# Optimization experiments

Measured on AMD Instinct MI355X. Metric: run time of the kernel, lower is better.

The kernel has to match this reference:

```python
import jax, jax.numpy as jnp
import numpy as np

N_NODES = 50000
N_EDGES = 800000
IN_FEAT = 256
DIM_H = 64
DIM_OUT = 64


def setup_inputs() -> dict:
    key = jax.random.key(0)
    ks = jax.random.split(key, 9)
    x = jax.random.normal(ks[0], (N_NODES, IN_FEAT), dtype=jnp.float32)
    edge_index = jax.random.randint(ks[1], (2, N_EDGES), 0, N_NODES, dtype=jnp.int64)
    s_in = 1.0 / np.sqrt(IN_FEAT)
    s_h = 1.0 / np.sqrt(DIM_H)
    W_src = jax.random.normal(ks[2], (IN_FEAT, DIM_H), dtype=jnp.float32) * s_in
    W_dst = jax.random.normal(ks[3], (IN_FEAT, DIM_H), dtype=jnp.float32) * s_in
    att_src = jax.random.normal(ks[4], (DIM_H,), dtype=jnp.float32) * s_h
    att_dst = jax.random.normal(ks[5], (DIM_H,), dtype=jnp.float32) * s_h
    bias_conv = jax.random.normal(ks[6], (DIM_H,), dtype=jnp.float32) * 0.01
    W_lin = jax.random.normal(ks[7], (DIM_H, DIM_OUT), dtype=jnp.float32) * s_h
    b_lin = jax.random.normal(ks[8], (DIM_OUT,), dtype=jnp.float32) * 0.01
    return {"x": x, "edge_index": edge_index, "W_src": W_src, "W_dst": W_dst,
            "att_src": att_src, "att_dst": att_dst, "bias_conv": bias_conv,
            "W_lin": W_lin, "b_lin": b_lin}


def reference(x, edge_index, W_src, W_dst, att_src, att_dst, bias_conv, W_lin, b_lin):
    N = x.shape[0]
    src, dst = edge_index[0], edge_index[1]
    # linear projections (GATConv lin_src / lin_dst, no bias)
    h_src = x @ W_src                      # [N, H]
    h_dst = x @ W_dst                      # [N, H]
    # per-node attention logits
    a_src = h_src @ att_src                # [N]
    a_dst = h_dst @ att_dst                # [N]
    # edge-wise score: leaky_relu(a_src[src] + a_dst[dst])
    e = jax.nn.leaky_relu(a_src[src] + a_dst[dst], negative_slope=0.2)  # [E]
    # segment softmax over destination neighborhoods
    e_max = jax.ops.segment_max(e, dst, num_segments=N)
    e_exp = jnp.exp(e - e_max[dst])
    denom = jax.ops.segment_sum(e_exp, dst, num_segments=N)
    alpha = e_exp / denom[dst]             # [E]
    # weighted scatter-add aggregation
    msg = h_src[src] * alpha[:, None]      # [E, H]
    out = jax.ops.segment_sum(msg, dst, num_segments=N) + bias_conv  # [N, H]
    h = jax.nn.relu(out)
    return h @ W_lin + b_lin               # [N, dim_out]
```

## Files before the change

### kernel.cpp

```cpp
#include <hip/hip_runtime.h>
#include <math.h>

#define N_NODES 50000
#define N_EDGES 800000
#define IN_FEAT 256
#define DIM_H   64
#define NPAD    50176
#define CAP     48
#define NBUK    392
#define BNODES  128
#define BCAP    3072
#define EPB     4096
#define PBLKS   391
#define ABLKS   196
#define SPLIT   4
#define PNODES  32

typedef __attribute__((ext_vector_type(8)))  short  s16x8;
typedef __attribute__((ext_vector_type(16))) float  f32x16;

__device__ __forceinline__ float bcast_f(float v, int k) {
  return __int_as_float(__builtin_amdgcn_readlane(__float_as_int(v), k));
}
__device__ __forceinline__ short f2bf(float f) {
  unsigned u = __float_as_uint(f);
  u += 0x7fffu + ((u >> 16) & 1u);
  return (short)(u >> 16);
}

__global__ __launch_bounds__(256) void proj_binA_kernel(
    const float* __restrict__ x,
    const float* __restrict__ Wsrc,
    const float* __restrict__ Wdst,
    const float* __restrict__ att_src,
    const float* __restrict__ att_dst,
    const int* __restrict__ ei,
    unsigned* __restrict__ hbf,
    float* __restrict__ a_src,
    float* __restrict__ a_dst,
    int* __restrict__ gbc,
    unsigned* __restrict__ binbuf) {
  __shared__ short wfrag[16 * 2 * 64 * 8];
  __shared__ float wdl[IN_FEAT];
  __shared__ float attl[DIM_H];

  const int tid = threadIdx.x;

  if (blockIdx.x >= PBLKS) {
    int* bcnt = (int*)wfrag;
    int* wcur = bcnt + NBUK;
    const int e0 = (blockIdx.x - PBLKS) * EPB;

    for (int b = tid; b < NBUK; b += 256) bcnt[b] = 0;
    __syncthreads();

    int dst[16];
    #pragma unroll
    for (int i = 0; i < 16; ++i) {
      int e = e0 + tid + 256 * i;
      dst[i] = (e < N_EDGES) ? ei[N_EDGES + e] : -1;
      if (dst[i] >= 0) atomicAdd(&bcnt[dst[i] >> 7], 1);
    }
    __syncthreads();

    for (int b = tid; b < NBUK; b += 256) {
      int c = bcnt[b];
      wcur[b] = c ? atomicAdd(&gbc[b], c) : 0;
    }
    __syncthreads();

    #pragma unroll
    for (int i = 0; i < 16; ++i) {
      int e = e0 + tid + 256 * i;
      if (e < N_EDGES) {
        int s = ei[e];
        int b = dst[i] >> 7;
        int pos = atomicAdd(&wcur[b], 1);
        if (pos < BCAP)
          binbuf[(long)b * BCAP + pos] =
              (unsigned)s | ((unsigned)(dst[i] & 127) << 16);
      }
    }
    return;
  }

  const int lane = tid & 63;
  const int wv   = tid >> 6;

  if (tid < DIM_H) attl[tid] = att_dst[tid];
  __syncthreads();

  {
    float s = 0.f;
    const float4* row = (const float4*)(Wdst + (long)tid * DIM_H);
    #pragma unroll
    for (int q = 0; q < 16; ++q) {
      float4 r = row[q];
      s = fmaf(r.x, attl[4 * q + 0], s);
      s = fmaf(r.y, attl[4 * q + 1], s);
      s = fmaf(r.z, attl[4 * q + 2], s);
      s = fmaf(r.w, attl[4 * q + 3], s);
    }
    wdl[tid] = s;
  }

  for (int e = tid; e < IN_FEAT * DIM_H; e += 256) {
    int k = e >> 6, n = e & 63;
    int s = k >> 4, half = (k >> 3) & 1, j = k & 7, t = n >> 5;
    int fl = (n & 31) + 32 * half;
    wfrag[((s * 2 + t) * 64 + fl) * 8 + j] = f2bf(Wsrc[e]);
  }
  __syncthreads();

  s16x8 bfr[32];
  #pragma unroll
  for (int f = 0; f < 32; ++f)
    bfr[f] = *(const s16x8*)(wfrag + (f * 64 + lane) * 8);

  const int base = (blockIdx.x * 4 + wv) * 32;
  int row = base + (lane & 31); if (row > N_NODES - 1) row = N_NODES - 1;
  const int koff = (lane >> 5) * 8;
  const float* px = x + (long)row * IN_FEAT + koff;

  f32x16 acc0 = {0.f}, acc1 = {0.f};
  #pragma unroll
  for (int i = 0; i < 16; ++i) { acc0[i] = 0.f; acc1[i] = 0.f; }
  float pd = 0.f;

  #pragma unroll
  for (int s = 0; s < 16; ++s) {
    float4 va = *(const float4*)(px + s * 16);
    float4 vb = *(const float4*)(px + s * 16 + 4);
    float4 w1 = *(const float4*)(wdl + s * 16 + koff);
    float4 w2 = *(const float4*)(wdl + s * 16 + koff + 4);
    pd = fmaf(va.x, w1.x, pd); pd = fmaf(va.y, w1.y, pd);
    pd = fmaf(va.z, w1.z, pd); pd = fmaf(va.w, w1.w, pd);
    pd = fmaf(vb.x, w2.x, pd); pd = fmaf(vb.y, w2.y, pd);
    pd = fmaf(vb.z, w2.z, pd); pd = fmaf(vb.w, w2.w, pd);
    s16x8 a;
    a[0] = f2bf(va.x); a[1] = f2bf(va.y); a[2] = f2bf(va.z); a[3] = f2bf(va.w);
    a[4] = f2bf(vb.x); a[5] = f2bf(vb.y); a[6] = f2bf(vb.z); a[7] = f2bf(vb.w);
    acc0 = __builtin_amdgcn_mfma_f32_32x32x16_bf16(a, bfr[s * 2 + 0], acc0, 0, 0, 0);
    acc1 = __builtin_amdgcn_mfma_f32_32x32x16_bf16(a, bfr[s * 2 + 1], acc1, 0, 0, 0);
  }

  const int col = lane & 31;
  const int rhi = 4 * (lane >> 5);

  #pragma unroll
  for (int r = 0; r < 16; ++r) {
    int node = base + (r & 3) + 8 * (r >> 2) + rhi;
    if (node < N_NODES) {
      unsigned p = (unsigned)(unsigned short)f2bf(acc0[r]) |
                   ((unsigned)(unsigned short)f2bf(acc1[r]) << 16);
      hbf[(long)node * 32 + col] = p;
    }
  }

  float att0 = att_src[col];
  float att1 = att_src[col + 32];
  #pragma unroll
  for (int r = 0; r < 16; ++r) {
    float t = acc0[r] * att0 + acc1[r] * att1;
    t += __shfl_xor(t, 1, 64);
    t += __shfl_xor(t, 2, 64);
    t += __shfl_xor(t, 4, 64);
    t += __shfl_xor(t, 8, 64);
    t += __shfl_xor(t, 16, 64);
    int node = base + (r & 3) + 8 * (r >> 2) + rhi;
    if (col == 0 && node < N_NODES) a_src[node] = t;
  }

  float pds = pd + __shfl_xor(pd, 32, 64);
  int node = base + (lane & 31);
  if (lane < 32 && node < N_NODES) a_dst[node] = pds;
}

__global__ __launch_bounds__(256) void gatherfused_kernel(
    const unsigned* __restrict__ binbuf,
    const int* __restrict__ gbc,
    const float* __restrict__ a_src,
    const float* __restrict__ a_dst,
    const unsigned* __restrict__ hbf,
    const float* __restrict__ bias_conv,
    const float* __restrict__ W_lin,
    const float* __restrict__ b_lin,
    float* __restrict__ out) {
  __shared__ unsigned rec[PNODES * CAP];
  __shared__ int   lcnt[PNODES];
  __shared__ float adl[PNODES];
  __shared__ float wl[64 * 64];

  const int tid    = threadIdx.x;
  const int bucket = blockIdx.x >> 2;
  const int part   = blockIdx.x & 3;
  const int nb     = bucket * BNODES + part * PNODES;
  const int dlo    = part * PNODES;

  for (int i = tid; i < 4096; i += 256) wl[i] = W_lin[i];
  if (tid < PNODES) {
    lcnt[tid] = 0;
    adl[tid]  = a_dst[nb + tid];
  }
  __syncthreads();

  int count = gbc[bucket]; if (count > BCAP) count = BCAP;
  const unsigned* bb = binbuf + (long)bucket * BCAP;
  for (int i = tid; i < count; i += 256) {
    unsigned u = bb[i];
    int dl = (int)(u >> 16) - dlo;
    if ((unsigned)dl < PNODES) {
      int s = (int)(u & 0xffffu);
      float sc = a_src[s] + adl[dl];
      sc = sc >= 0.f ? sc : 0.2f * sc;
      float w = __expf(sc);
      int pos = atomicAdd(&lcnt[dl], 1);
      if (pos < CAP)
        rec[dl * CAP + pos] =
            ((unsigned)(unsigned short)f2bf(w) << 16) | (u & 0xffffu);
    }
  }
  __syncthreads();

  const int lane = tid & 63;
  const int wv   = __builtin_amdgcn_readfirstlane(tid >> 6);
  const int grp8 = lane >> 3;
  const int ql8  = lane & 7;
  const float bj  = bias_conv[lane];
  const float blj = b_lin[lane];

  for (int q = 0; q < 8; ++q) {
    const int dl = wv * 8 + q;
    const int n  = nb + dl;
    int m = lcnt[dl]; if (m > CAP) m = CAP;

    float alo[4] = {0.f, 0.f, 0.f, 0.f};
    float ahi[4] = {0.f, 0.f, 0.f, 0.f};
    float den = 0.f;

    for (int j = 0; j < m; j += 8) {
      int idx = j + grp8;
      int ci = idx < m ? idx : m - 1;
      unsigned u = rec[dl * CAP + ci];
      float w = __uint_as_float(u & 0xffff0000u);
      if (idx >= m) w = 0.f;
      int s_e = (int)(u & 0xffffu);
      uint4 hp = *(const uint4*)(hbf + (long)s_e * 32 + ql8 * 4);
      alo[0] = fmaf(w, __uint_as_float(hp.x << 16),         alo[0]);
      ahi[0] = fmaf(w, __uint_as_float(hp.x & 0xffff0000u), ahi[0]);
      alo[1] = fmaf(w, __uint_as_float(hp.y << 16),         alo[1]);
      ahi[1] = fmaf(w, __uint_as_float(hp.y & 0xffff0000u), ahi[1]);
      alo[2] = fmaf(w, __uint_as_float(hp.z << 16),         alo[2]);
      ahi[2] = fmaf(w, __uint_as_float(hp.z & 0xffff0000u), ahi[2]);
      alo[3] = fmaf(w, __uint_as_float(hp.w << 16),         alo[3]);
      ahi[3] = fmaf(w, __uint_as_float(hp.w & 0xffff0000u), ahi[3]);
      den += w;
    }

    #pragma unroll
    for (int mm = 8; mm <= 32; mm <<= 1) {
      #pragma unroll
      for (int c = 0; c < 4; ++c) {
        alo[c] += __shfl_xor(alo[c], mm, 64);
        ahi[c] += __shfl_xor(ahi[c], mm, 64);
      }
      den += __shfl_xor(den, mm, 64);
    }
    int srcl = (lane & 31) >> 2;
    float v0 = __shfl(alo[0], srcl, 64);
    float v1 = __shfl(alo[1], srcl, 64);
    float v2 = __shfl(alo[2], srcl, 64);
    float v3 = __shfl(alo[3], srcl, 64);
    float v4 = __shfl(ahi[0], srcl, 64);
    float v5 = __shfl(ahi[1], srcl, 64);
    float v6 = __shfl(ahi[2], srcl, 64);
    float v7 = __shfl(ahi[3], srcl, 64);
    int c4 = lane & 3;
    float losel = (c4 == 0) ? v0 : (c4 == 1) ? v1 : (c4 == 2) ? v2 : v3;
    float hisel = (c4 == 0) ? v4 : (c4 == 1) ? v5 : (c4 == 2) ? v6 : v7;
    float accl = (lane >> 5) ? hisel : losel;

    float inv = den > 0.f ? 1.0f / den : 0.f;
    float z = fmaf(accl, inv, bj);
    float h = fmaxf(z, 0.f);
    float o = blj;
    #pragma unroll
    for (int k = 0; k < 64; ++k)
      o = fmaf(bcast_f(h, k), wl[k * 64 + lane], o);
    if (n < N_NODES) out[(long)n * DIM_H + lane] = o;
  }
}

extern "C" void kernel_launch(void* const* d_in, const int* in_sizes, int n_in,
                              void* d_out, int out_size, void* d_ws, size_t ws_size,
                              hipStream_t stream) {
  const float* x        = (const float*)d_in[0];
  const int*   ei       = (const int*)d_in[1];
  const float* Wsrc     = (const float*)d_in[2];
  const float* Wdst     = (const float*)d_in[3];
  const float* att_src  = (const float*)d_in[4];
  const float* att_dst  = (const float*)d_in[5];
  const float* bias_cv  = (const float*)d_in[6];
  const float* W_lin    = (const float*)d_in[7];
  const float* b_lin    = (const float*)d_in[8];
  float* out = (float*)d_out;

  unsigned* hbf    = (unsigned*)d_ws;
  float*    a_src  = (float*)(hbf + 1600000);
  float*    a_dst  = a_src + NPAD;
  int*      gbc    = (int*)(a_dst + NPAD);
  unsigned* binbuf = (unsigned*)(gbc + 512);

  hipMemsetAsync(gbc, 0, 512 * sizeof(int), stream);

  proj_binA_kernel<<<PBLKS + ABLKS, 256, 0, stream>>>(
      x, Wsrc, Wdst, att_src, att_dst, ei, hbf, a_src, a_dst, gbc, binbuf);

  gatherfused_kernel<<<NBUK * SPLIT, 256, 0, stream>>>(
      binbuf, gbc, a_src, a_dst, hbf, bias_cv, W_lin, b_lin, out);
}
```

Before: 189.3 us.

## Split gather buckets finer, hoist x loads, unroll gather and output dot

The fused gather kernel now splits each 128-node bucket into 8 parts of 16 nodes instead of 4 of 32. That doubles the block count, and each block rescans the whole bucket's edge list, filtering to its own destinations. The gather loop handles two edges per iteration so two hbf loads are in flight at once, and the final 64x64 linear uses four independent accumulators to break the FMA dependency chain. In the projection kernel, all x loads are issued up front and weight fragments are read from LDS per step instead of held in 32 registers, trading register pressure for memory-level parallelism.

Measured after the change: 197.5 us. +4.4%, slower.

```diff
diff --git a/kernel.cpp b/kernel.cpp
--- a/kernel.cpp
+++ b/kernel.cpp
@@ -13,8 +13,8 @@
 #define EPB     4096
 #define PBLKS   391
 #define ABLKS   196
-#define SPLIT   4
-#define PNODES  32
+#define SPLIT   8
+#define PNODES  16
 
 typedef __attribute__((ext_vector_type(8)))  short  s16x8;
 typedef __attribute__((ext_vector_type(16))) float  f32x16;
@@ -112,36 +112,40 @@
   }
   __syncthreads();
 
-  s16x8 bfr[32];
-  #pragma unroll
-  for (int f = 0; f < 32; ++f)
-    bfr[f] = *(const s16x8*)(wfrag + (f * 64 + lane) * 8);
-
   const int base = (blockIdx.x * 4 + wv) * 32;
   int row = base + (lane & 31); if (row > N_NODES - 1) row = N_NODES - 1;
   const int koff = (lane >> 5) * 8;
   const float* px = x + (long)row * IN_FEAT + koff;
 
-  f32x16 acc0 = {0.f}, acc1 = {0.f};
+  float4 va[16], vb[16];
+  #pragma unroll
+  for (int s = 0; s < 16; ++s) {
+    va[s] = *(const float4*)(px + s * 16);
+    vb[s] = *(const float4*)(px + s * 16 + 4);
+  }
+
+  f32x16 acc0, acc1;
   #pragma unroll
   for (int i = 0; i < 16; ++i) { acc0[i] = 0.f; acc1[i] = 0.f; }
   float pd = 0.f;
 
   #pragma unroll
   for (int s = 0; s < 16; ++s) {
-    float4 va = *(const float4*)(px + s * 16);
-    float4 vb = *(const float4*)(px + s * 16 + 4);
     float4 w1 = *(const float4*)(wdl + s * 16 + koff);
     float4 w2 = *(const float4*)(wdl + s * 16 + koff + 4);
-    pd = fmaf(va.x, w1.x, pd); pd = fmaf(va.y, w1.y, pd);
-    pd = fmaf(va.z, w1.z, pd); pd = fmaf(va.w, w1.w, pd);
-    pd = fmaf(vb.x, w2.x, pd); pd = fmaf(vb.y, w2.y, pd);
-    pd = fmaf(vb.z, w2.z, pd); pd = fmaf(vb.w, w2.w, pd);
+    pd = fmaf(va[s].x, w1.x, pd); pd = fmaf(va[s].y, w1.y, pd);
+    pd = fmaf(va[s].z, w1.z, pd); pd = fmaf(va[s].w, w1.w, pd);
+    pd = fmaf(vb[s].x, w2.x, pd); pd = fmaf(vb[s].y, w2.y, pd);
+    pd = fmaf(vb[s].z, w2.z, pd); pd = fmaf(vb[s].w, w2.w, pd);
     s16x8 a;
-    a[0] = f2bf(va.x); a[1] = f2bf(va.y); a[2] = f2bf(va.z); a[3] = f2bf(va.w);
-    a[4] = f2bf(vb.x); a[5] = f2bf(vb.y); a[6] = f2bf(vb.z); a[7] = f2bf(vb.w);
-    acc0 = __builtin_amdgcn_mfma_f32_32x32x16_bf16(a, bfr[s * 2 + 0], acc0, 0, 0, 0);
-    acc1 = __builtin_amdgcn_mfma_f32_32x32x16_bf16(a, bfr[s * 2 + 1], acc1, 0, 0, 0);
+    a[0] = f2bf(va[s].x); a[1] = f2bf(va[s].y);
+    a[2] = f2bf(va[s].z); a[3] = f2bf(va[s].w);
+    a[4] = f2bf(vb[s].x); a[5] = f2bf(vb[s].y);
+    a[6] = f2bf(vb[s].z); a[7] = f2bf(vb[s].w);
+    s16x8 b0 = *(const s16x8*)(wfrag + ((s * 2 + 0) * 64 + lane) * 8);
+    s16x8 b1 = *(const s16x8*)(wfrag + ((s * 2 + 1) * 64 + lane) * 8);
+    acc0 = __builtin_amdgcn_mfma_f32_32x32x16_bf16(a, b0, acc0, 0, 0, 0);
+    acc1 = __builtin_amdgcn_mfma_f32_32x32x16_bf16(a, b1, acc1, 0, 0, 0);
   }
 
   const int col = lane & 31;
@@ -192,8 +196,8 @@
   __shared__ float wl[64 * 64];
 
   const int tid    = threadIdx.x;
-  const int bucket = blockIdx.x >> 2;
-  const int part   = blockIdx.x & 3;
+  const int bucket = blockIdx.x >> 3;
+  const int part   = blockIdx.x & 7;
   const int nb     = bucket * BNODES + part * PNODES;
   const int dlo    = part * PNODES;
 
@@ -229,8 +233,8 @@
   const float bj  = bias_conv[lane];
   const float blj = b_lin[lane];
 
-  for (int q = 0; q < 8; ++q) {
-    const int dl = wv * 8 + q;
+  for (int q = 0; q < 4; ++q) {
+    const int dl = wv * 4 + q;
     const int n  = nb + dl;
     int m = lcnt[dl]; if (m > CAP) m = CAP;
 
@@ -238,23 +242,39 @@
     float ahi[4] = {0.f, 0.f, 0.f, 0.f};
     float den = 0.f;
 
-    for (int j = 0; j < m; j += 8) {
-      int idx = j + grp8;
-      int ci = idx < m ? idx : m - 1;
-      unsigned u = rec[dl * CAP + ci];
-      float w = __uint_as_float(u & 0xffff0000u);
-      if (idx >= m) w = 0.f;
-      int s_e = (int)(u & 0xffffu);
-      uint4 hp = *(const uint4*)(hbf + (long)s_e * 32 + ql8 * 4);
-      alo[0] = fmaf(w, __uint_as_float(hp.x << 16),         alo[0]);
-      ahi[0] = fmaf(w, __uint_as_float(hp.x & 0xffff0000u), ahi[0]);
-      alo[1] = fmaf(w, __uint_as_float(hp.y << 16),         alo[1]);
-      ahi[1] = fmaf(w, __uint_as_float(hp.y & 0xffff0000u), ahi[1]);
-      alo[2] = fmaf(w, __uint_as_float(hp.z << 16),         alo[2]);
-      ahi[2] = fmaf(w, __uint_as_float(hp.z & 0xffff0000u), ahi[2]);
-      alo[3] = fmaf(w, __uint_as_float(hp.w << 16),         alo[3]);
-      ahi[3] = fmaf(w, __uint_as_float(hp.w & 0xffff0000u), ahi[3]);
-      den += w;
+    for (int j = 0; j < m; j += 16) {
+      int idx0 = j + grp8;
+      int idx1 = j + 8 + grp8;
+      int ci0 = idx0 < m ? idx0 : m - 1;
+      int ci1 = idx1 < m ? idx1 : m - 1;
+      unsigned u0 = rec[dl * CAP + ci0];
+      unsigned u1 = rec[dl * CAP + ci1];
+      float w0 = __uint_as_float(u0 & 0xffff0000u);
+      float w1 = __uint_as_float(u1 & 0xffff0000u);
+      if (idx0 >= m) w0 = 0.f;
+      if (idx1 >= m) w1 = 0.f;
+      int s0 = (int)(u0 & 0xffffu);
+      int s1 = (int)(u1 & 0xffffu);
+      uint4 hp0 = *(const uint4*)(hbf + (long)s0 * 32 + ql8 * 4);
+      uint4 hp1 = *(const uint4*)(hbf + (long)s1 * 32 + ql8 * 4);
+      alo[0] = fmaf(w0, __uint_as_float(hp0.x << 16),         alo[0]);
+      ahi[0] = fmaf(w0, __uint_as_float(hp0.x & 0xffff0000u), ahi[0]);
+      alo[1] = fmaf(w0, __uint_as_float(hp0.y << 16),         alo[1]);
+      ahi[1] = fmaf(w0, __uint_as_float(hp0.y & 0xffff0000u), ahi[1]);
+      alo[2] = fmaf(w0, __uint_as_float(hp0.z << 16),         alo[2]);
+      ahi[2] = fmaf(w0, __uint_as_float(hp0.z & 0xffff0000u), ahi[2]);
+      alo[3] = fmaf(w0, __uint_as_float(hp0.w << 16),         alo[3]);
+      ahi[3] = fmaf(w0, __uint_as_float(hp0.w & 0xffff0000u), ahi[3]);
+      den += w0;
+      alo[0] = fmaf(w1, __uint_as_float(hp1.x << 16),         alo[0]);
+      ahi[0] = fmaf(w1, __uint_as_float(hp1.x & 0xffff0000u), ahi[0]);
+      alo[1] = fmaf(w1, __uint_as_float(hp1.y << 16),         alo[1]);
+      ahi[1] = fmaf(w1, __uint_as_float(hp1.y & 0xffff0000u), ahi[1]);
+      alo[2] = fmaf(w1, __uint_as_float(hp1.z << 16),         alo[2]);
+      ahi[2] = fmaf(w1, __uint_as_float(hp1.z & 0xffff0000u), ahi[2]);
+      alo[3] = fmaf(w1, __uint_as_float(hp1.w << 16),         alo[3]);
+      ahi[3] = fmaf(w1, __uint_as_float(hp1.w & 0xffff0000u), ahi[3]);
+      den += w1;
     }
 
     #pragma unroll
@@ -283,10 +303,15 @@
     float inv = den > 0.f ? 1.0f / den : 0.f;
     float z = fmaf(accl, inv, bj);
     float h = fmaxf(z, 0.f);
-    float o = blj;
-    #pragma unroll
-    for (int k = 0; k < 64; ++k)
-      o = fmaf(bcast_f(h, k), wl[k * 64 + lane], o);
+    float o0 = blj, o1 = 0.f, o2 = 0.f, o3 = 0.f;
+    #pragma unroll
+    for (int k = 0; k < 64; k += 4) {
+      o0 = fmaf(bcast_f(h, k + 0), wl[(k + 0) * 64 + lane], o0);
+      o1 = fmaf(bcast_f(h, k + 1), wl[(k + 1) * 64 + lane], o1);
+      o2 = fmaf(bcast_f(h, k + 2), wl[(k + 2) * 64 + lane], o2);
+      o3 = fmaf(bcast_f(h, k + 3), wl[(k + 3) * 64 + lane], o3);
+    }
+    float o = (o0 + o1) + (o2 + o3);
     if (n < N_NODES) out[(long)n * DIM_H + lane] = o;
   }
 }
```
